# Kernel optimization log

Hardware: AMD Instinct MI355X
Metric: run time of the kernel (lower is better)

## Reference

```python
import jax, jax.numpy as jnp
import numpy as np

B, H, N_CHAR, MAX_LEN = 512, 1024, 128, 256


def setup_inputs() -> dict:
    key = jax.random.key(0)
    ks = jax.random.split(key, 8)
    s = 1.0 / np.sqrt(H)  # PyTorch LSTMCell/Linear uniform init scale
    hid = jax.random.normal(ks[0], (B, H), dtype=jnp.float32)
    cell0 = jax.random.normal(ks[1], (B, H), dtype=jnp.float32)
    # constant start-token one-hot input (input0_tensor in the original)
    inp0 = jnp.zeros((B, N_CHAR), dtype=jnp.float32).at[:, 0].set(1.0)
    W_ih = jax.random.uniform(ks[2], (4 * H, N_CHAR + H), jnp.float32, -s, s)
    W_hh = jax.random.uniform(ks[3], (4 * H, H), jnp.float32, -s, s)
    b_ih = jax.random.uniform(ks[4], (4 * H,), jnp.float32, -s, s)
    b_hh = jax.random.uniform(ks[5], (4 * H,), jnp.float32, -s, s)
    W_out = jax.random.uniform(ks[6], (N_CHAR, H), jnp.float32, -s, s)
    b_out = jax.random.uniform(ks[7], (N_CHAR,), jnp.float32, -s, s)
    return {"hid": hid, "inp0": inp0, "cell0": cell0,
            "W_ih": W_ih, "W_hh": W_hh, "b_ih": b_ih, "b_hh": b_hh,
            "W_out": W_out, "b_out": b_out}


def reference(hid, inp0, cell0, W_ih, W_hh, b_ih, b_hh, W_out, b_out):
    # x_t = concat(inp0, h) is constant in its first N_CHAR columns, so
    # precompute inp0's contribution once (same math as cat + single GEMM).
    x_part = inp0 @ W_ih[:, :N_CHAR].T + b_ih + b_hh  # (B, 4H)
    W_ih_h = W_ih[:, N_CHAR:]  # (4H, H) acting on h

    def step(carry, _):
        h, c = carry
        gates = x_part + h @ W_ih_h.T + h @ W_hh.T  # (B, 4H)
        i, f, g, o = jnp.split(gates, 4, axis=1)  # PyTorch gate order i,f,g,o
        c = jax.nn.sigmoid(f) * c + jax.nn.sigmoid(i) * jnp.tanh(g)
        h = jax.nn.sigmoid(o) * jnp.tanh(c)
        return (h, c), h @ W_out.T + b_out  # logits (B, N_CHAR)

    _, outs = jax.lax.scan(step, (hid, cell0), None, length=MAX_LEN)
    # outs: (max_len, B, N_CHAR) -> (B, N_CHAR, max_len) to match torch.stack(dim=2)
    return jnp.transpose(outs, (1, 2, 0))
```

## Files before the change

kernel.cpp:

```cpp
#include <hip/hip_runtime.h>
#include <hip/hip_bf16.h>


using bf16 = __hip_bfloat16;
typedef short bf16x8 __attribute__((ext_vector_type(8)));
typedef float f32x4  __attribute__((ext_vector_type(4)));
typedef float f32x16 __attribute__((ext_vector_type(16)));

static constexpr int BATCH = 512;
static constexpr int HID   = 1024;
static constexpr int NCH   = 128;
static constexpr int TLEN  = 256;
static constexpr int NP    = 4096;

static constexpr size_t OFF_WP  = 0;
static constexpr size_t OFF_WOB = OFF_WP  + (size_t)NP * HID * 2;
static constexpr size_t OFF_HB0 = OFF_WOB + (size_t)NCH * HID * 2;
static constexpr size_t OFF_HB1 = OFF_HB0 + (size_t)BATCH * HID * 2;
static constexpr size_t OFF_XP  = OFF_HB1 + (size_t)BATCH * HID * 2;
static constexpr size_t OFF_BAR = OFF_XP  + (size_t)BATCH * NP * 4;

__device__ __forceinline__ float sigm(float x) { return 1.f / (1.f + __expf(-x)); }

__device__ __forceinline__ unsigned short f2bf(float x) {
  unsigned u = __float_as_uint(x);
  return (unsigned short)((u + 0x7FFFu + ((u >> 16) & 1u)) >> 16);
}

__device__ __forceinline__ int rowp_to_n(int rp) {
  int jg = rp >> 6, c = rp & 63;
  return (c >> 4) * HID + jg * 16 + (c & 15);
}

__global__ void prep_misc(const float* __restrict__ hid0, const float* __restrict__ wout,
                          bf16* __restrict__ hb0, bf16* __restrict__ wob,
                          unsigned* __restrict__ bar)
{
  int gid = blockIdx.x * blockDim.x + threadIdx.x;
  int stride = gridDim.x * blockDim.x;
  for (int i = gid; i < BATCH * HID; i += stride) hb0[i] = __float2bfloat16(hid0[i]);
  for (int i = gid; i < NCH * HID;  i += stride) wob[i] = __float2bfloat16(wout[i]);
  if (gid < 1024) bar[gid] = 0u;
}

__global__ void prep_wp(const float* __restrict__ W_ih, const float* __restrict__ W_hh,
                        bf16* __restrict__ wp)
{
  int gid = blockIdx.x * blockDim.x + threadIdx.x;
  int stride = gridDim.x * blockDim.x;
  for (int i = gid; i < NP * HID; i += stride) {
    int rp = i >> 10, k = i & 1023;
    int n = rowp_to_n(rp);
    float v = W_ih[(size_t)n * 1152 + 128 + k] + W_hh[(size_t)n * 1024 + k];
    wp[i] = __float2bfloat16(v);
  }
}

__global__ void prep_xp(const float* __restrict__ inp0, const float* __restrict__ W_ih,
                        const float* __restrict__ b_ih, const float* __restrict__ b_hh,
                        float* __restrict__ xp)
{
  int b = blockIdx.x;
  const float4* ip = (const float4*)(inp0 + b * NCH);
  for (int rp = threadIdx.x; rp < NP; rp += blockDim.x) {
    int n = rowp_to_n(rp);
    const float4* wr = (const float4*)(W_ih + (size_t)n * 1152);
    float acc = b_ih[n] + b_hh[n];
    #pragma unroll 8
    for (int q = 0; q < 32; ++q) {
      float4 a = ip[q], w = wr[q];
      acc += a.x * w.x + a.y * w.y + a.z * w.z + a.w * w.w;
    }
    xp[(size_t)b * NP + rp] = acc;
  }
}

__launch_bounds__(256, 1)
__global__ void lstm_main(const bf16* __restrict__ wp, const bf16* __restrict__ wob,
                          const float* __restrict__ xp, const float* __restrict__ cell0,
                          const float* __restrict__ bout,
                          bf16* __restrict__ hb0, bf16* __restrict__ hb1,
                          float* __restrict__ out, unsigned* __restrict__ bar)
{
  __shared__ bf16 wlds[64 * HID];
  __shared__ float obuf[16][16][17];
  __shared__ float opart[3][16][16];
  __shared__ int s_pop[8];

  const int tid  = threadIdx.x;
  const int bx   = blockIdx.x;
  const int lane = tid & 63;
  const int wv   = tid >> 6;
  const int bm   = bx >> 6;
  const int jg   = bx & 63;
  const int wrow = bm * 128 + wv * 32;
  const int l31  = lane & 31;
  const int lhi  = lane >> 5;
  const bool low = (l31 < 16);
  const int jj   = lane & 15;
  const int jcol = jg * 16 + jj;

  {
    const char* src = (const char*)(wp + (size_t)jg * 64 * HID);
    for (int it = tid; it < 8192; it += 256) {
      int r  = it >> 7;
      int kb = (it & 127) << 4;
      bf16x8 v = *(const bf16x8*)(src + r * 2048 + kb);
      *(bf16x8*)((char*)wlds + r * 2048 + (kb ^ ((r & 15) << 4))) = v;
    }
  }

  f32x16 xpA, xpB;
  #pragma unroll
  for (int q = 0; q < 16; ++q) {
    int rr = (q & 3) + ((q >> 2) << 3) + (lhi << 2);
    const float* xr = xp + (size_t)(wrow + rr) * NP + jg * 64;
    xpA[q] = xr[l31];
    xpB[q] = xr[32 + l31];
  }

  float creg[8];
  #pragma unroll
  for (int q = 0; q < 8; ++q) {
    int rr = (q & 3) + ((q >> 2) << 3) + (lhi << 2) + (low ? 0 : 16);
    creg[q] = cell0[(size_t)(wrow + rr) * HID + jcol];
  }

  const int omt = (bx >> 3) << 4;
  const int ont = (bx & 7) << 4;
  const float bo = bout[ont + jj];

  const int myx = __builtin_amdgcn_s_getreg(6164) & 7;
  if (tid == 0) {
    __hip_atomic_fetch_add(bar + (size_t)myx * 32, 1u, __ATOMIC_RELAXED, __HIP_MEMORY_SCOPE_AGENT);
    __threadfence();
    __hip_atomic_fetch_add(bar + (size_t)8 * 32, 1u, __ATOMIC_RELEASE, __HIP_MEMORY_SCOPE_AGENT);
    int it = 0;
    while (__hip_atomic_load(bar + (size_t)8 * 32, __ATOMIC_RELAXED, __HIP_MEMORY_SCOPE_AGENT) < 256u) {
      __builtin_amdgcn_s_sleep(1);
      if ((++it & 255) == 0) __builtin_amdgcn_fence(__ATOMIC_ACQUIRE, "agent");
    }
  }
  __syncthreads();
  if (tid < 8)
    s_pop[tid] = (int)__hip_atomic_load(bar + (size_t)tid * 32, __ATOMIC_RELAXED, __HIP_MEMORY_SCOPE_AGENT);
  __syncthreads();
  int nx = 0, tot = 0;
  #pragma unroll
  for (int i = 0; i < 8; ++i) { nx += (s_pop[i] != 0) ? 1 : 0; tot += s_pop[i]; }
  const bool elect = (nx >= 2) && (tot == 256);
  const unsigned mypop = (unsigned)s_pop[myx];
  const unsigned NF = elect ? (unsigned)nx : 256u;
  unsigned* const xcdCnt = bar + (size_t)(16 + myx) * 32;
  unsigned* const gCnt   = bar + (size_t)24 * 32;
  unsigned* const epochX = bar + (size_t)(800 + myx * 16);

  __syncthreads();

  for (int t = 0; t <= TLEN + 1; ++t) {
    const bf16* __restrict__ hcur = (t & 1) ? hb1 : hb0;
    bf16* __restrict__ hnxt = (t & 1) ? hb0 : hb1;

    if (t >= 17 && ((t - 17) & 15) == 0) {
      const int orow = tid >> 4, ocol = tid & 15;
      float* dst = out + ((size_t)(omt + orow) * NCH + (ont + ocol)) * TLEN + (t - 17);
      #pragma unroll
      for (int s = 0; s < 16; ++s) dst[s] = obuf[orow][ocol][s];
    }

    bool lastx = false;
    if (t < TLEN) {
      f32x16 accA = xpA, accB = xpB;
      {
        const bf16* ap = hcur + (size_t)(wrow + l31) * HID + (lhi << 3);
        const char* wb = (const char*)wlds;
        const int base0 = l31 * 2048;
        const int sxor  = (l31 & 15) << 4;
        const int kb4   = lhi << 4;
        #pragma unroll 16
        for (int ks = 0; ks < 64; ++ks) {
          bf16x8 av = *(const bf16x8*)(ap + ks * 16);
          const int ko = ((ks << 5) | kb4) ^ sxor;
          bf16x8 b0 = *(const bf16x8*)(wb + base0 + ko);
          bf16x8 b1 = *(const bf16x8*)(wb + base0 + 65536 + ko);
          accA = __builtin_amdgcn_mfma_f32_32x32x16_bf16(av, b0, accA, 0, 0, 0);
          accB = __builtin_amdgcn_mfma_f32_32x32x16_bf16(av, b1, accB, 0, 0, 0);
        }
      }

      float s0[16], s1[16], u0[16], u1[16];
      #pragma unroll
      for (int q = 0; q < 16; ++q) {
        s0[q] = sigm(accA[q]);
        float a1 = accB[q];
        float sg = sigm(low ? 2.f * a1 : a1);
        s1[q] = low ? 2.f * sg - 1.f : sg;
      }
      #pragma unroll
      for (int q = 0; q < 16; ++q) {
        u0[q] = __shfl_xor(s0[q], 16);
        u1[q] = __shfl_xor(s1[q], 16);
      }

      {
        unsigned* const h32 = (unsigned*)hnxt;
        #pragma unroll
        for (int q = 0; q < 8; ++q) {
          float fg  = low ? u0[q]         : s0[q + 8];
          float ig  = low ? s0[q] * s1[q] : u0[q + 8] * u1[q + 8];
          float og  = low ? u1[q]         : s1[q + 8];
          float cn  = fg * creg[q] + ig;
          creg[q] = cn;
          float hv = og * (2.f * sigm(2.f * cn) - 1.f);
          unsigned v = (unsigned)f2bf(hv);
          unsigned p = (unsigned)__shfl_xor((int)v, 1);
          if (!(lane & 1)) {
            int rr = (q & 3) + ((q >> 2) << 3) + (lhi << 2) + (low ? 0 : 16);
            __hip_atomic_store(&h32[((size_t)(wrow + rr) << 9) + (jcol >> 1)],
                               v | (p << 16), __ATOMIC_RELAXED, __HIP_MEMORY_SCOPE_AGENT);
          }
        }
      }

      asm volatile("s_waitcnt vmcnt(0)" ::: "memory");
      __syncthreads();
      if (tid == 0) {
        unsigned old = __hip_atomic_fetch_add(xcdCnt, 1u, __ATOMIC_RELAXED, __HIP_MEMORY_SCOPE_AGENT);
        lastx = !elect || (old == mypop * (unsigned)(t + 1) - 1u);
        if (lastx) {
          if (elect) {
            __hip_atomic_fetch_add(gCnt, 1u, __ATOMIC_RELAXED, __HIP_MEMORY_SCOPE_AGENT);
          } else {
            __threadfence();
            __hip_atomic_fetch_add(gCnt, 1u, __ATOMIC_RELEASE, __HIP_MEMORY_SCOPE_AGENT);
          }
        }
      }
    }

    if (t >= 1 && t <= TLEN && wv > 0) {
      f32x4 oacc = {0.f, 0.f, 0.f, 0.f};
      const int kq = (lane >> 4) << 3;
      const bf16* ap2 = hcur + (size_t)(omt + jj) * HID + kq;
      const bf16* bp2 = wob + (size_t)(ont + jj) * HID + kq;
      const int k0 = (wv - 1) * 11;
      const int k1 = (k0 + 11 < 32) ? k0 + 11 : 32;
      #pragma unroll 4
      for (int ks = k0; ks < k1; ++ks) {
        bf16x8 avv = *(const bf16x8*)(ap2 + ks * 32);
        bf16x8 bvv = *(const bf16x8*)(bp2 + ks * 32);
        oacc = __builtin_amdgcn_mfma_f32_16x16x32_bf16(avv, bvv, oacc, 0, 0, 0);
      }
      #pragma unroll
      for (int q = 0; q < 4; ++q)
        opart[wv - 1][((lane >> 4) << 2) + q][jj] = oacc[q];
    }

    if (t < TLEN && tid == 0) {
      if (!elect) {
        const unsigned tgt = NF * (unsigned)(t + 1);
        int it = 0;
        while (__hip_atomic_load(gCnt, __ATOMIC_RELAXED, __HIP_MEMORY_SCOPE_AGENT) < tgt) {
          __builtin_amdgcn_s_sleep(1);
          if ((++it & 255) == 0) __builtin_amdgcn_fence(__ATOMIC_ACQUIRE, "agent");
        }
      } else if (lastx) {
        const unsigned tgt = (unsigned)nx * (unsigned)(t + 1);
        int it = 0;
        while (__hip_atomic_load(gCnt, __ATOMIC_RELAXED, __HIP_MEMORY_SCOPE_AGENT) < tgt) {
          __builtin_amdgcn_s_sleep(1);
          if ((++it & 255) == 0) __builtin_amdgcn_fence(__ATOMIC_ACQUIRE, "agent");
        }
        __builtin_amdgcn_fence(__ATOMIC_ACQUIRE, "agent");
        __hip_atomic_store(epochX, (unsigned)(t + 1), __ATOMIC_RELAXED, __HIP_MEMORY_SCOPE_AGENT);
      } else {
        const unsigned want = (unsigned)(t + 1);
        int it = 0; bool ok = false;
        while (true) {
          if (__hip_atomic_load(epochX, __ATOMIC_RELAXED, __HIP_MEMORY_SCOPE_AGENT) >= want) { ok = true; break; }
          __builtin_amdgcn_s_sleep(1);
          if (++it > (1 << 18)) break;
        }
        if (ok) {
          asm volatile("buffer_inv" ::: "memory");
        } else {
          const unsigned tgt = (unsigned)nx * (unsigned)(t + 1);
          int it2 = 0;
          while (__hip_atomic_load(gCnt, __ATOMIC_RELAXED, __HIP_MEMORY_SCOPE_AGENT) < tgt) {
            __builtin_amdgcn_s_sleep(1);
            if ((++it2 & 255) == 0) __builtin_amdgcn_fence(__ATOMIC_ACQUIRE, "agent");
          }
          __threadfence();
        }
      }
    }
    if (t < TLEN && !elect && tid < 64) __builtin_amdgcn_fence(__ATOMIC_ACQUIRE, "agent");
    __syncthreads();

    if (t >= 1 && t <= TLEN) {
      const int orow = tid >> 4, ocol = tid & 15;
      float s = opart[0][orow][ocol] + opart[1][orow][ocol] + opart[2][orow][ocol];
      obuf[orow][ocol][(t - 1) & 15] = s + bo;
    }
    __syncthreads();
  }
}

extern "C" void kernel_launch(void* const* d_in, const int* in_sizes, int n_in,
                              void* d_out, int out_size, void* d_ws, size_t ws_size,
                              hipStream_t stream)
{
  const float* hid0  = (const float*)d_in[0];
  const float* inp0  = (const float*)d_in[1];
  const float* cell0 = (const float*)d_in[2];
  const float* W_ih  = (const float*)d_in[3];
  const float* W_hh  = (const float*)d_in[4];
  const float* b_ih  = (const float*)d_in[5];
  const float* b_hh  = (const float*)d_in[6];
  const float* W_out = (const float*)d_in[7];
  const float* b_out = (const float*)d_in[8];
  float* out = (float*)d_out;

  char* ws = (char*)d_ws;
  bf16* wp      = (bf16*)(ws + OFF_WP);
  bf16* wob     = (bf16*)(ws + OFF_WOB);
  bf16* hb0     = (bf16*)(ws + OFF_HB0);
  bf16* hb1     = (bf16*)(ws + OFF_HB1);
  float* xp     = (float*)(ws + OFF_XP);
  unsigned* bar = (unsigned*)(ws + OFF_BAR);

  prep_misc<<<512, 256, 0, stream>>>(hid0, W_out, hb0, wob, bar);
  prep_wp<<<4096, 256, 0, stream>>>(W_ih, W_hh, wp);
  prep_xp<<<512, 256, 0, stream>>>(inp0, W_ih, b_ih, b_hh, xp);

  void* args[] = { &wp, &wob, &xp, &cell0, &b_out, &hb0, &hb1, &out, &bar };
  hipError_t e = hipLaunchCooperativeKernel(lstm_main, dim3(256), dim3(256), args, 0u, stream);
  if (e != hipSuccess) {
    lstm_main<<<dim3(256), dim3(256), 0, stream>>>(wp, wob, xp, cell0, b_out,
                                                   hb0, hb1, out, bar);
  }
}
```

Before: 3.777 ms.

## Stage h tile in LDS for vector stores and simplify grid barrier to global counter polling

Each block now writes its new hidden-state values into a shared-memory tile and issues one 16-byte global store per thread with an sc1 cache hint, replacing per-lane packed 32-bit atomic stores. The hierarchical barrier that had per-XCD leaders publish an epoch flag is removed. All blocks now poll the global counter directly, and per-XCD last arrivers do a buffer_inv before incrementing it. The aim is fewer, wider stores and a shorter barrier critical path. The cost is an extra __syncthreads per step, more contention on the single global counter, and memory-ordering changes that rely on cache-invalidate semantics.

```diff
diff --git a/kernel.cpp b/kernel.cpp
--- a/kernel.cpp
+++ b/kernel.cpp
@@ -21,11 +21,6 @@
 static constexpr size_t OFF_BAR = OFF_XP  + (size_t)BATCH * NP * 4;
 
 __device__ __forceinline__ float sigm(float x) { return 1.f / (1.f + __expf(-x)); }
-
-__device__ __forceinline__ unsigned short f2bf(float x) {
-  unsigned u = __float_as_uint(x);
-  return (unsigned short)((u + 0x7FFFu + ((u >> 16) & 1u)) >> 16);
-}
 
 __device__ __forceinline__ int rowp_to_n(int rp) {
   int jg = rp >> 6, c = rp & 63;
@@ -85,6 +80,7 @@
   __shared__ bf16 wlds[64 * HID];
   __shared__ float obuf[16][16][17];
   __shared__ float opart[3][16][16];
+  __shared__ bf16 htile[128][24];
   __shared__ int s_pop[8];
 
   const int tid  = threadIdx.x;
@@ -130,6 +126,10 @@
   const int ont = (bx & 7) << 4;
   const float bo = bout[ont + jj];
 
+  const int prow  = tid >> 1;
+  const int phalf = tid & 1;
+  char* const pdst0 = (char*)0 + ((size_t)(bm * 128 + prow) * HID + jg * 16 + phalf * 8) * 2;
+
   const int myx = __builtin_amdgcn_s_getreg(6164) & 7;
   if (tid == 0) {
     __hip_atomic_fetch_add(bar + (size_t)myx * 32, 1u, __ATOMIC_RELAXED, __HIP_MEMORY_SCOPE_AGENT);
@@ -153,7 +153,6 @@
   const unsigned NF = elect ? (unsigned)nx : 256u;
   unsigned* const xcdCnt = bar + (size_t)(16 + myx) * 32;
   unsigned* const gCnt   = bar + (size_t)24 * 32;
-  unsigned* const epochX = bar + (size_t)(800 + myx * 16);
 
   __syncthreads();
 
@@ -168,7 +167,6 @@
       for (int s = 0; s < 16; ++s) dst[s] = obuf[orow][ocol][s];
     }
 
-    bool lastx = false;
     if (t < TLEN) {
       f32x16 accA = xpA, accB = xpB;
       {
@@ -201,41 +199,39 @@
         u0[q] = __shfl_xor(s0[q], 16);
         u1[q] = __shfl_xor(s1[q], 16);
       }
+      #pragma unroll
+      for (int q = 0; q < 8; ++q) {
+        float fg  = low ? u0[q]         : s0[q + 8];
+        float ig  = low ? s0[q] * s1[q] : u0[q + 8] * u1[q + 8];
+        float og  = low ? u1[q]         : s1[q + 8];
+        float cn  = fg * creg[q] + ig;
+        creg[q] = cn;
+        float hv = og * (2.f * sigm(2.f * cn) - 1.f);
+        int rr = (q & 3) + ((q >> 2) << 3) + (lhi << 2) + (low ? 0 : 16);
+        htile[wv * 32 + rr][jj] = __float2bfloat16(hv);
+      }
+      __syncthreads();
 
       {
-        unsigned* const h32 = (unsigned*)hnxt;
-        #pragma unroll
-        for (int q = 0; q < 8; ++q) {
-          float fg  = low ? u0[q]         : s0[q + 8];
-          float ig  = low ? s0[q] * s1[q] : u0[q + 8] * u1[q + 8];
-          float og  = low ? u1[q]         : s1[q + 8];
-          float cn  = fg * creg[q] + ig;
-          creg[q] = cn;
-          float hv = og * (2.f * sigm(2.f * cn) - 1.f);
-          unsigned v = (unsigned)f2bf(hv);
-          unsigned p = (unsigned)__shfl_xor((int)v, 1);
-          if (!(lane & 1)) {
-            int rr = (q & 3) + ((q >> 2) << 3) + (lhi << 2) + (low ? 0 : 16);
-            __hip_atomic_store(&h32[((size_t)(wrow + rr) << 9) + (jcol >> 1)],
-                               v | (p << 16), __ATOMIC_RELAXED, __HIP_MEMORY_SCOPE_AGENT);
-          }
-        }
-      }
-
+        bf16x8 vv = *(const bf16x8*)(&htile[prow][phalf * 8]);
+        char* dst = (char*)hnxt + (size_t)(pdst0 - (char*)0);
+        asm volatile("global_store_dwordx4 %0, %1, off sc1" :: "v"(dst), "v"(vv) : "memory");
+      }
       asm volatile("s_waitcnt vmcnt(0)" ::: "memory");
       __syncthreads();
+
       if (tid == 0) {
         unsigned old = __hip_atomic_fetch_add(xcdCnt, 1u, __ATOMIC_RELAXED, __HIP_MEMORY_SCOPE_AGENT);
-        lastx = !elect || (old == mypop * (unsigned)(t + 1) - 1u);
+        const bool lastx = elect && (old == mypop * (unsigned)(t + 1) - 1u);
         if (lastx) {
-          if (elect) {
-            __hip_atomic_fetch_add(gCnt, 1u, __ATOMIC_RELAXED, __HIP_MEMORY_SCOPE_AGENT);
-          } else {
-            __threadfence();
-            __hip_atomic_fetch_add(gCnt, 1u, __ATOMIC_RELEASE, __HIP_MEMORY_SCOPE_AGENT);
-          }
+          asm volatile("buffer_inv sc1\n\ts_waitcnt vmcnt(0)" ::: "memory");
+          __hip_atomic_fetch_add(gCnt, 1u, __ATOMIC_RELAXED, __HIP_MEMORY_SCOPE_AGENT);
+        } else if (!elect) {
+          __threadfence();
+          __hip_atomic_fetch_add(gCnt, 1u, __ATOMIC_RELEASE, __HIP_MEMORY_SCOPE_AGENT);
         }
       }
+      if (elect && wv == 0) asm volatile("buffer_inv" ::: "memory");
     }
 
     if (t >= 1 && t <= TLEN && wv > 0) {
@@ -257,41 +253,11 @@
     }
 
     if (t < TLEN && tid == 0) {
-      if (!elect) {
-        const unsigned tgt = NF * (unsigned)(t + 1);
-        int it = 0;
-        while (__hip_atomic_load(gCnt, __ATOMIC_RELAXED, __HIP_MEMORY_SCOPE_AGENT) < tgt) {
-          __builtin_amdgcn_s_sleep(1);
-          if ((++it & 255) == 0) __builtin_amdgcn_fence(__ATOMIC_ACQUIRE, "agent");
-        }
-      } else if (lastx) {
-        const unsigned tgt = (unsigned)nx * (unsigned)(t + 1);
-        int it = 0;
-        while (__hip_atomic_load(gCnt, __ATOMIC_RELAXED, __HIP_MEMORY_SCOPE_AGENT) < tgt) {
-          __builtin_amdgcn_s_sleep(1);
-          if ((++it & 255) == 0) __builtin_amdgcn_fence(__ATOMIC_ACQUIRE, "agent");
-        }
-        __builtin_amdgcn_fence(__ATOMIC_ACQUIRE, "agent");
-        __hip_atomic_store(epochX, (unsigned)(t + 1), __ATOMIC_RELAXED, __HIP_MEMORY_SCOPE_AGENT);
-      } else {
-        const unsigned want = (unsigned)(t + 1);
-        int it = 0; bool ok = false;
-        while (true) {
-          if (__hip_atomic_load(epochX, __ATOMIC_RELAXED, __HIP_MEMORY_SCOPE_AGENT) >= want) { ok = true; break; }
-          __builtin_amdgcn_s_sleep(1);
-          if (++it > (1 << 18)) break;
-        }
-        if (ok) {
-          asm volatile("buffer_inv" ::: "memory");
-        } else {
-          const unsigned tgt = (unsigned)nx * (unsigned)(t + 1);
-          int it2 = 0;
-          while (__hip_atomic_load(gCnt, __ATOMIC_RELAXED, __HIP_MEMORY_SCOPE_AGENT) < tgt) {
-            __builtin_amdgcn_s_sleep(1);
-            if ((++it2 & 255) == 0) __builtin_amdgcn_fence(__ATOMIC_ACQUIRE, "agent");
-          }
-          __threadfence();
-        }
+      const unsigned tgt = NF * (unsigned)(t + 1);
+      int it = 0;
+      while (__hip_atomic_load(gCnt, __ATOMIC_RELAXED, __HIP_MEMORY_SCOPE_AGENT) < tgt) {
+        __builtin_amdgcn_s_sleep(1);
+        if ((++it & 1023) == 0) __builtin_amdgcn_fence(__ATOMIC_ACQUIRE, "agent");
       }
     }
     if (t < TLEN && !elect && tid < 64) __builtin_amdgcn_fence(__ATOMIC_ACQUIRE, "agent");
```

Result: slower. 3.930 ms (+4.1%).
